# Optimization experiments

Hardware: AMD Instinct MI355X
Metric: run time of the kernel (lower is better)

Reference implementation:

```python
import jax, jax.numpy as jnp
import numpy as np

B, S, UNITS = 64, 2048, 1024


def setup_inputs() -> dict:
    key = jax.random.key(0)
    ks = jax.random.split(key, 6)
    scale = 1.0 / np.sqrt(UNITS)
    return {
        "s_prev": jax.random.normal(ks[0], (B, UNITS), dtype=jnp.float32),
        "hidden_states": jax.random.normal(ks[1], (B, S, UNITS), dtype=jnp.float32),
        "W_w": jax.random.normal(ks[2], (UNITS, UNITS), dtype=jnp.float32) * scale,
        "W_b": jnp.zeros((UNITS,), dtype=jnp.float32),
        "U_w": jax.random.normal(ks[3], (UNITS, UNITS), dtype=jnp.float32) * scale,
        "U_b": jnp.zeros((UNITS,), dtype=jnp.float32),
        "V_w": jax.random.normal(ks[4], (UNITS, 1), dtype=jnp.float32) * scale,
        "V_b": jnp.zeros((1,), dtype=jnp.float32),
    }


def reference(s_prev, hidden_states, W_w, W_b, U_w, U_b, V_w, V_b):
    # W(s_prev): [B, units] -> [B, 1, units]
    W_s = (s_prev @ W_w + W_b)[:, None, :]
    # U(hidden_states): [B, S, units]
    U_h = jnp.einsum('bsu,uk->bsk', hidden_states, U_w) + U_b
    # V(tanh(W_s + U_h)): [B, S, 1]
    scores = jnp.tanh(W_s + U_h) @ V_w + V_b
    # softmax over seq axis
    weights = jax.nn.softmax(scores, axis=1)  # [B, S, 1]
    # weighted sum over seq -> context [B, units]
    context = jnp.sum(weights * hidden_states, axis=1)
    return context, weights
```

## Files before the change

kernel.cpp:

```cpp
#include <hip/hip_runtime.h>

#define BB   64
#define SS   2048
#define UU   1024
#define MM   (BB * SS)

typedef unsigned short u16;
typedef unsigned int   u32;
typedef __attribute__((ext_vector_type(8))) short bf16x8;
typedef __attribute__((ext_vector_type(4))) float f32x4;

__device__ __forceinline__ u16 f2b(float f) {
    u32 x = __float_as_uint(f);
    u32 r = (x + 0x7fffu + ((x >> 16) & 1u)) >> 16;
    return (u16)r;
}
__device__ __forceinline__ float b2f(u16 u) {
    return __uint_as_float(((u32)u) << 16);
}
__device__ __forceinline__ float fast_tanh(float x) {
    x = fminf(fmaxf(x, -15.f), 15.f);
    float e = __expf(2.f * x);
    return (e - 1.f) / (e + 1.f);
}
__device__ __forceinline__ void async_copy16(const u16* gp, u16* lp) {
    __builtin_amdgcn_global_load_lds(
        (const __attribute__((address_space(1))) unsigned int*)gp,
        (__attribute__((address_space(3))) unsigned int*)lp, 16, 0, 0);
}

__global__ __launch_bounds__(256) void k_transpose_uw(const float* __restrict__ Uw,
                                                      u16* __restrict__ UwT) {
    __shared__ float tile[64][65];
    int n0 = blockIdx.x * 64, k0 = blockIdx.y * 64;
    int c = threadIdx.x & 63, r0 = threadIdx.x >> 6;
#pragma unroll
    for (int i = 0; i < 64; i += 4)
        tile[r0 + i][c] = Uw[(size_t)(k0 + r0 + i) * UU + n0 + c];
    __syncthreads();
#pragma unroll
    for (int i = 0; i < 64; i += 4)
        UwT[(size_t)(n0 + r0 + i) * UU + k0 + c] = f2b(tile[c][r0 + i]);
}

__global__ __launch_bounds__(256) void k_convert_h(const float* __restrict__ src,
                                                   u16* __restrict__ dst) {
    size_t i = ((size_t)blockIdx.x * 256 + threadIdx.x) * 8;
    float4 f0 = *(const float4*)(src + i);
    float4 f1 = *(const float4*)(src + i + 4);
    u16 t[8];
    t[0] = f2b(f0.x); t[1] = f2b(f0.y); t[2] = f2b(f0.z); t[3] = f2b(f0.w);
    t[4] = f2b(f1.x); t[5] = f2b(f1.y); t[6] = f2b(f1.z); t[7] = f2b(f1.w);
    *(uint4*)(dst + i) = *(uint4*)t;
}

__global__ __launch_bounds__(256) void k_ws(const float* __restrict__ sp,
                                            const float* __restrict__ Ww,
                                            const float* __restrict__ Wb,
                                            float* __restrict__ Ws) {
    int u = blockIdx.x * 256 + threadIdx.x;
    int b = blockIdx.y;
    int k0 = blockIdx.z * 256;
    const float* sprow = sp + (size_t)b * UU + k0;
    float acc = (blockIdx.z == 0) ? Wb[u] : 0.f;
#pragma unroll 4
    for (int k = 0; k < 256; ++k)
        acc = fmaf(sprow[k], Ww[(size_t)(k0 + k) * UU + u], acc);
    atomicAdd(&Ws[(size_t)b * UU + u], acc);
}

__global__ __launch_bounds__(256) void k_gemm_lds(const u16* __restrict__ A,
                                                  const u16* __restrict__ UwT,
                                                  const float* __restrict__ Ws,
                                                  const float* __restrict__ Ub,
                                                  const float* __restrict__ Vw,
                                                  float* __restrict__ scp) {
    __shared__ __align__(16) u16 As[128 * 64];
    __shared__ __align__(16) u16 Bs[128 * 64];
    const int tid  = threadIdx.x;
    const int lane = tid & 63;
    const int wave = tid >> 6;
    const int wm = wave >> 1, wn = wave & 1;
    const int quad = lane >> 4, l15 = lane & 15;

    const int bid = blockIdx.x;
    const int g   = bid >> 6;
    const int mt  = g * 8 + (bid & 7);
    const int nt  = (bid >> 3) & 7;
    const int n0  = nt * 128;
    const size_t m0 = (size_t)mt * 128;

    const int srow   = lane >> 3;
    const int schunk = (lane & 7) ^ srow;
    const size_t lane_off = (size_t)srow * UU + (size_t)schunk * 8;

    f32x4 acc[4][4];
#pragma unroll
    for (int i = 0; i < 4; ++i)
#pragma unroll
        for (int j = 0; j < 4; ++j) acc[i][j] = (f32x4){0.f, 0.f, 0.f, 0.f};

    for (int kk = 0; kk < UU; kk += 64) {
#pragma unroll
        for (int i = 0; i < 4; ++i) {
            const int gi = wave * 4 + i;
            async_copy16(A + (m0 + gi * 8) * UU + kk + lane_off, As + gi * 512);
        }
#pragma unroll
        for (int i = 0; i < 4; ++i) {
            const int gi = wave * 4 + i;
            async_copy16(UwT + (size_t)(n0 + gi * 8) * UU + kk + lane_off, Bs + gi * 512);
        }
        __syncthreads();
#pragma unroll
        for (int k2 = 0; k2 < 2; ++k2) {
            const int chunk = quad + k2 * 4;
            const int pos = chunk ^ (l15 & 7);
            bf16x8 a[4], b[4];
#pragma unroll
            for (int mi = 0; mi < 4; ++mi) {
                int r = wm * 64 + mi * 16 + l15;
                a[mi] = *(const bf16x8*)(As + r * 64 + pos * 8);
            }
#pragma unroll
            for (int ni = 0; ni < 4; ++ni) {
                int r = wn * 64 + ni * 16 + l15;
                b[ni] = *(const bf16x8*)(Bs + r * 64 + pos * 8);
            }
#pragma unroll
            for (int mi = 0; mi < 4; ++mi)
#pragma unroll
                for (int ni = 0; ni < 4; ++ni)
                    acc[mi][ni] = __builtin_amdgcn_mfma_f32_16x16x32_bf16(
                        a[mi], b[ni], acc[mi][ni], 0, 0, 0);
        }
        __syncthreads();
    }

    const int bidx = (int)(m0 >> 11);
    const float* wsrow = Ws + (size_t)bidx * UU;
    float wsv[4], ubv[4], vwv[4];
#pragma unroll
    for (int ni = 0; ni < 4; ++ni) {
        int ng = n0 + wn * 64 + ni * 16 + l15;
        wsv[ni] = wsrow[ng];
        ubv[ni] = Ub[ng];
        vwv[ni] = Vw[ng];
    }
#pragma unroll
    for (int mi = 0; mi < 4; ++mi) {
#pragma unroll
        for (int r = 0; r < 4; ++r) {
            float v = 0.f;
#pragma unroll
            for (int ni = 0; ni < 4; ++ni) {
                float x = acc[mi][ni][r] + wsv[ni] + ubv[ni];
                v = fmaf(fast_tanh(x), vwv[ni], v);
            }
#pragma unroll
            for (int off = 1; off < 16; off <<= 1)
                v += __shfl_xor(v, off, 64);
            if (l15 == 0) {
                size_t mg = m0 + wm * 64 + mi * 16 + quad * 4 + r;
                scp[mg * 16 + nt * 2 + wn] = v;
            }
        }
    }
}

__global__ __launch_bounds__(256) void k_gemm_f32(const float* __restrict__ Aptr,
                                                  const u16* __restrict__ UwT,
                                                  const float* __restrict__ Ws,
                                                  const float* __restrict__ Ub,
                                                  const float* __restrict__ Vw,
                                                  float* __restrict__ scp) {
    __shared__ __align__(16) u16 As[128][72];
    __shared__ __align__(16) u16 Bs[128][72];
    const int tid  = threadIdx.x;
    const int lane = tid & 63;
    const int wave = tid >> 6;
    const int wm = wave >> 1, wn = wave & 1;
    const int quad = lane >> 4, l15 = lane & 15;
    const int nt = blockIdx.x;
    const int n0 = nt * 128;
    const size_t m0 = (size_t)blockIdx.y * 128;

    f32x4 acc[4][4];
#pragma unroll
    for (int i = 0; i < 4; ++i)
#pragma unroll
        for (int j = 0; j < 4; ++j) acc[i][j] = (f32x4){0.f, 0.f, 0.f, 0.f};

    const int sr = tid >> 3;
    const int sc = (tid & 7) * 8;

    for (int kk = 0; kk < UU; kk += 64) {
#pragma unroll
        for (int i = 0; i < 4; ++i) {
            int r = sr + i * 32;
            const float4* p = (const float4*)(Aptr + (m0 + r) * UU + kk + sc);
            float4 f0 = p[0], f1 = p[1];
            u16 t[8];
            t[0] = f2b(f0.x); t[1] = f2b(f0.y); t[2] = f2b(f0.z); t[3] = f2b(f0.w);
            t[4] = f2b(f1.x); t[5] = f2b(f1.y); t[6] = f2b(f1.z); t[7] = f2b(f1.w);
            *(uint4*)(&As[r][sc]) = *(uint4*)t;
        }
#pragma unroll
        for (int i = 0; i < 4; ++i) {
            int r = sr + i * 32;
            uint4 v = *(const uint4*)(UwT + (size_t)(n0 + r) * UU + kk + sc);
            *(uint4*)(&Bs[r][sc]) = v;
        }
        __syncthreads();
#pragma unroll
        for (int k2 = 0; k2 < 64; k2 += 32) {
            bf16x8 a[4], b[4];
#pragma unroll
            for (int mi = 0; mi < 4; ++mi)
                a[mi] = *(const bf16x8*)(&As[wm * 64 + mi * 16 + l15][k2 + quad * 8]);
#pragma unroll
            for (int ni = 0; ni < 4; ++ni)
                b[ni] = *(const bf16x8*)(&Bs[wn * 64 + ni * 16 + l15][k2 + quad * 8]);
#pragma unroll
            for (int mi = 0; mi < 4; ++mi)
#pragma unroll
                for (int ni = 0; ni < 4; ++ni)
                    acc[mi][ni] = __builtin_amdgcn_mfma_f32_16x16x32_bf16(
                        a[mi], b[ni], acc[mi][ni], 0, 0, 0);
        }
        __syncthreads();
    }

    const int bidx = (int)(m0 >> 11);
    const float* wsrow = Ws + (size_t)bidx * UU;
    float wsv[4], ubv[4], vwv[4];
#pragma unroll
    for (int ni = 0; ni < 4; ++ni) {
        int ng = n0 + wn * 64 + ni * 16 + l15;
        wsv[ni] = wsrow[ng];
        ubv[ni] = Ub[ng];
        vwv[ni] = Vw[ng];
    }
#pragma unroll
    for (int mi = 0; mi < 4; ++mi) {
#pragma unroll
        for (int r = 0; r < 4; ++r) {
            float v = 0.f;
#pragma unroll
            for (int ni = 0; ni < 4; ++ni) {
                float x = acc[mi][ni][r] + wsv[ni] + ubv[ni];
                v = fmaf(fast_tanh(x), vwv[ni], v);
            }
#pragma unroll
            for (int off = 1; off < 16; off <<= 1)
                v += __shfl_xor(v, off, 64);
            if (l15 == 0) {
                size_t mg = m0 + wm * 64 + mi * 16 + quad * 4 + r;
                scp[mg * 16 + nt * 2 + wn] = v;
            }
        }
    }
}

__global__ __launch_bounds__(256) void k_softmax(const float* __restrict__ scp,
                                                 float* __restrict__ wout) {
    int b = blockIdx.x, t = threadIdx.x;
    __shared__ float red[256];
    float sc[8];
    float lmax = -1e30f;
#pragma unroll
    for (int i = 0; i < 8; ++i) {
        int s = t + i * 256;
        const float4* p = (const float4*)(scp + ((size_t)b * SS + s) * 16);
        float4 a = p[0], c = p[1], d = p[2], e = p[3];
        float v = (a.x + a.y + a.z + a.w) + (c.x + c.y + c.z + c.w) +
                  (d.x + d.y + d.z + d.w) + (e.x + e.y + e.z + e.w);
        sc[i] = v;
        lmax = fmaxf(lmax, v);
    }
    red[t] = lmax;
    __syncthreads();
    for (int o = 128; o > 0; o >>= 1) {
        if (t < o) red[t] = fmaxf(red[t], red[t + o]);
        __syncthreads();
    }
    float mx = red[0];
    __syncthreads();
    float lsum = 0.f;
#pragma unroll
    for (int i = 0; i < 8; ++i) {
        sc[i] = __expf(sc[i] - mx);
        lsum += sc[i];
    }
    red[t] = lsum;
    __syncthreads();
    for (int o = 128; o > 0; o >>= 1) {
        if (t < o) red[t] += red[t + o];
        __syncthreads();
    }
    float inv = 1.f / red[0];
#pragma unroll
    for (int i = 0; i < 8; ++i)
        wout[(size_t)b * SS + t + i * 256] = sc[i] * inv;
}

template <bool HBF16>
__global__ __launch_bounds__(256) void k_context(const void* __restrict__ hptr,
                                                 const float* __restrict__ w,
                                                 float* __restrict__ ctx) {
    int b = blockIdx.y;
    int s0 = blockIdx.x * 128;
    int u = threadIdx.x * 4;
    const float* wrow = w + (size_t)b * SS + s0;
    float a0 = 0.f, a1 = 0.f, a2 = 0.f, a3 = 0.f;
    for (int i = 0; i < 128; ++i) {
        float wv = wrow[i];
        size_t base = ((size_t)b * SS + s0 + i) * UU + u;
        if (HBF16) {
            ushort4 hv = *(const ushort4*)((const u16*)hptr + base);
            a0 = fmaf(wv, b2f(hv.x), a0);
            a1 = fmaf(wv, b2f(hv.y), a1);
            a2 = fmaf(wv, b2f(hv.z), a2);
            a3 = fmaf(wv, b2f(hv.w), a3);
        } else {
            float4 hv = *(const float4*)((const float*)hptr + base);
            a0 = fmaf(wv, hv.x, a0);
            a1 = fmaf(wv, hv.y, a1);
            a2 = fmaf(wv, hv.z, a2);
            a3 = fmaf(wv, hv.w, a3);
        }
    }
    atomicAdd(&ctx[(size_t)b * UU + u + 0], a0);
    atomicAdd(&ctx[(size_t)b * UU + u + 1], a1);
    atomicAdd(&ctx[(size_t)b * UU + u + 2], a2);
    atomicAdd(&ctx[(size_t)b * UU + u + 3], a3);
}

extern "C" void kernel_launch(void* const* d_in, const int* in_sizes, int n_in,
                              void* d_out, int out_size, void* d_ws, size_t ws_size,
                              hipStream_t stream) {
    const float* s_prev = (const float*)d_in[0];
    const float* h      = (const float*)d_in[1];
    const float* Ww     = (const float*)d_in[2];
    const float* Wb     = (const float*)d_in[3];
    const float* Uw     = (const float*)d_in[4];
    const float* Ub     = (const float*)d_in[5];
    const float* Vw     = (const float*)d_in[6];

    float* out = (float*)d_out;
    char* ws = (char*)d_ws;

    u16*   UwT = (u16*)ws;
    float* Ws  = (float*)(ws + (size_t)(2 << 20));
    float* scp = (float*)(ws + (size_t)(2 << 20) + (256 << 10));
    size_t offH = (size_t)(2 << 20) + (256 << 10) + ((size_t)8 << 20);
    u16*   hbf = (u16*)(ws + offH);
    const size_t hBytes = (size_t)MM * UU * 2;
    const bool useBf16 = (ws_size >= offH + hBytes);

    hipMemsetAsync(out, 0, (size_t)BB * UU * sizeof(float), stream);
    hipMemsetAsync(Ws, 0, (size_t)BB * UU * sizeof(float), stream);

    k_transpose_uw<<<dim3(16, 16), 256, 0, stream>>>(Uw, UwT);
    k_ws<<<dim3(4, BB, 4), 256, 0, stream>>>(s_prev, Ww, Wb, Ws);

    if (useBf16) {
        k_convert_h<<<(MM * (UU / 8)) / 256, 256, 0, stream>>>(h, hbf);
        k_gemm_lds<<<8192, 256, 0, stream>>>(hbf, UwT, Ws, Ub, Vw, scp);
    } else {
        k_gemm_f32<<<dim3(8, MM / 128), 256, 0, stream>>>(h, UwT, Ws, Ub, Vw, scp);
    }

    k_softmax<<<BB, 256, 0, stream>>>(scp, out + (size_t)BB * UU);

    if (useBf16)
        k_context<true><<<dim3(16, BB), 256, 0, stream>>>(hbf, out + (size_t)BB * UU, out);
    else
        k_context<false><<<dim3(16, BB), 256, 0, stream>>>(h, out + (size_t)BB * UU, out);
}
```

Baseline: 1.260 ms.

## Rewrite bf16 score GEMM as 256x256 tile with 4-stage async LDS pipeline

Replaces the 128x128 single-buffered GEMM with a 512-thread 256x256 tile kernel that uses a 4-deep ring of LDS buffers filled by async global-to-LDS copies, with explicit vmcnt waits and one barrier per k-step. Each wave now computes 128x64 of output. Blocks are remapped across XCDs, and the LDS swizzle is adapted to the 32-wide k chunks. The aim is to hide global load latency behind MFMA work and raise arithmetic intensity per loaded byte. The cost is much higher register and LDS use (128KB of LDS per block), which may limit occupancy.

```diff
diff --git a/kernel.cpp b/kernel.cpp
--- a/kernel.cpp
+++ b/kernel.cpp
@@ -28,6 +28,8 @@
         (const __attribute__((address_space(1))) unsigned int*)gp,
         (__attribute__((address_space(3))) unsigned int*)lp, 16, 0, 0);
 }
+
+#define WAITV(N) asm volatile("s_waitcnt vmcnt(" #N ")" ::: "memory")
 
 __global__ __launch_bounds__(256) void k_transpose_uw(const float* __restrict__ Uw,
                                                       u16* __restrict__ UwT) {
@@ -69,73 +71,96 @@
     atomicAdd(&Ws[(size_t)b * UU + u], acc);
 }
 
-__global__ __launch_bounds__(256) void k_gemm_lds(const u16* __restrict__ A,
-                                                  const u16* __restrict__ UwT,
-                                                  const float* __restrict__ Ws,
-                                                  const float* __restrict__ Ub,
-                                                  const float* __restrict__ Vw,
-                                                  float* __restrict__ scp) {
-    __shared__ __align__(16) u16 As[128 * 64];
-    __shared__ __align__(16) u16 Bs[128 * 64];
+__global__ __launch_bounds__(512, 2) void k_gemm256(const u16* __restrict__ A,
+                                                    const u16* __restrict__ UwT,
+                                                    const float* __restrict__ Ws,
+                                                    const float* __restrict__ Ub,
+                                                    const float* __restrict__ Vw,
+                                                    float* __restrict__ scp) {
+    __shared__ __align__(16) u16 As[4][8192];
+    __shared__ __align__(16) u16 Bs[4][8192];
     const int tid  = threadIdx.x;
     const int lane = tid & 63;
     const int wave = tid >> 6;
-    const int wm = wave >> 1, wn = wave & 1;
+    const int wm = wave >> 2;
+    const int wn = wave & 3;
     const int quad = lane >> 4, l15 = lane & 15;
 
     const int bid = blockIdx.x;
-    const int g   = bid >> 6;
-    const int mt  = g * 8 + (bid & 7);
-    const int nt  = (bid >> 3) & 7;
-    const int n0  = nt * 128;
-    const size_t m0 = (size_t)mt * 128;
-
-    const int srow   = lane >> 3;
-    const int schunk = (lane & 7) ^ srow;
+    const int xcd = bid & 7;
+    const int li  = bid >> 3;
+    const int mt  = xcd * 64 + (li >> 2);
+    const int nt  = li & 3;
+    const size_t m0 = (size_t)mt * 256;
+    const int n0  = nt * 256;
+
+    const int srow   = lane >> 2;
+    const int schunk = (lane & 3) ^ ((srow >> 1) & 3);
     const size_t lane_off = (size_t)srow * UU + (size_t)schunk * 8;
-
-    f32x4 acc[4][4];
-#pragma unroll
-    for (int i = 0; i < 4; ++i)
+    const int gA = wave * 2;
+
+    int offA[8], offB[4];
+#pragma unroll
+    for (int mi = 0; mi < 8; ++mi) {
+        int r = wm * 128 + mi * 16 + l15;
+        offA[mi] = r * 32 + (quad ^ ((r >> 1) & 3)) * 8;
+    }
+#pragma unroll
+    for (int ni = 0; ni < 4; ++ni) {
+        int r = wn * 64 + ni * 16 + l15;
+        offB[ni] = r * 32 + (quad ^ ((r >> 1) & 3)) * 8;
+    }
+
+    f32x4 acc[8][4];
+#pragma unroll
+    for (int i = 0; i < 8; ++i)
 #pragma unroll
         for (int j = 0; j < 4; ++j) acc[i][j] = (f32x4){0.f, 0.f, 0.f, 0.f};
 
-    for (int kk = 0; kk < UU; kk += 64) {
-#pragma unroll
-        for (int i = 0; i < 4; ++i) {
-            const int gi = wave * 4 + i;
-            async_copy16(A + (m0 + gi * 8) * UU + kk + lane_off, As + gi * 512);
-        }
-#pragma unroll
-        for (int i = 0; i < 4; ++i) {
-            const int gi = wave * 4 + i;
-            async_copy16(UwT + (size_t)(n0 + gi * 8) * UU + kk + lane_off, Bs + gi * 512);
-        }
-        __syncthreads();
-#pragma unroll
-        for (int k2 = 0; k2 < 2; ++k2) {
-            const int chunk = quad + k2 * 4;
-            const int pos = chunk ^ (l15 & 7);
-            bf16x8 a[4], b[4];
-#pragma unroll
-            for (int mi = 0; mi < 4; ++mi) {
-                int r = wm * 64 + mi * 16 + l15;
-                a[mi] = *(const bf16x8*)(As + r * 64 + pos * 8);
-            }
-#pragma unroll
-            for (int ni = 0; ni < 4; ++ni) {
-                int r = wn * 64 + ni * 16 + l15;
-                b[ni] = *(const bf16x8*)(Bs + r * 64 + pos * 8);
-            }
-#pragma unroll
-            for (int mi = 0; mi < 4; ++mi)
-#pragma unroll
-                for (int ni = 0; ni < 4; ++ni)
-                    acc[mi][ni] = __builtin_amdgcn_mfma_f32_16x16x32_bf16(
-                        a[mi], b[ni], acc[mi][ni], 0, 0, 0);
-        }
-        __syncthreads();
-    }
+    const u16* Abase = A + m0 * UU;
+    const u16* Bbase = UwT + (size_t)n0 * UU;
+
+#define STAGE(kt) do {                                                         \
+        const int _b = (kt) & 3;                                               \
+        const u16* _ga = Abase + (size_t)(gA * 16) * UU + (kt) * 32 + lane_off;\
+        async_copy16(_ga,                  &As[_b][gA * 512]);                 \
+        async_copy16(_ga + (size_t)16 * UU, &As[_b][(gA + 1) * 512]);          \
+        const u16* _gb = Bbase + (size_t)(gA * 16) * UU + (kt) * 32 + lane_off;\
+        async_copy16(_gb,                  &Bs[_b][gA * 512]);                 \
+        async_copy16(_gb + (size_t)16 * UU, &Bs[_b][(gA + 1) * 512]);          \
+    } while (0)
+
+    auto compute = [&](int kt) {
+        const u16* ab = As[kt & 3];
+        const u16* bb = Bs[kt & 3];
+        bf16x8 a[8], b[4];
+#pragma unroll
+        for (int mi = 0; mi < 8; ++mi) a[mi] = *(const bf16x8*)(ab + offA[mi]);
+#pragma unroll
+        for (int ni = 0; ni < 4; ++ni) b[ni] = *(const bf16x8*)(bb + offB[ni]);
+        __builtin_amdgcn_s_setprio(1);
+#pragma unroll
+        for (int mi = 0; mi < 8; ++mi)
+#pragma unroll
+            for (int ni = 0; ni < 4; ++ni)
+                acc[mi][ni] = __builtin_amdgcn_mfma_f32_16x16x32_bf16(
+                    a[mi], b[ni], acc[mi][ni], 0, 0, 0);
+        __builtin_amdgcn_s_setprio(0);
+    };
+
+    STAGE(0); STAGE(1); STAGE(2);
+
+    for (int kt = 0; kt < 29; ++kt) {
+        WAITV(8);
+        __builtin_amdgcn_sched_barrier(0);
+        __builtin_amdgcn_s_barrier();
+        STAGE(kt + 3);
+        compute(kt);
+    }
+    WAITV(8); __builtin_amdgcn_sched_barrier(0); __builtin_amdgcn_s_barrier(); compute(29);
+    WAITV(4); __builtin_amdgcn_sched_barrier(0); __builtin_amdgcn_s_barrier(); compute(30);
+    WAITV(0); __builtin_amdgcn_sched_barrier(0); __builtin_amdgcn_s_barrier(); compute(31);
+#undef STAGE
 
     const int bidx = (int)(m0 >> 11);
     const float* wsrow = Ws + (size_t)bidx * UU;
@@ -148,7 +173,7 @@
         vwv[ni] = Vw[ng];
     }
 #pragma unroll
-    for (int mi = 0; mi < 4; ++mi) {
+    for (int mi = 0; mi < 8; ++mi) {
 #pragma unroll
         for (int r = 0; r < 4; ++r) {
             float v = 0.f;
@@ -161,8 +186,8 @@
             for (int off = 1; off < 16; off <<= 1)
                 v += __shfl_xor(v, off, 64);
             if (l15 == 0) {
-                size_t mg = m0 + wm * 64 + mi * 16 + quad * 4 + r;
-                scp[mg * 16 + nt * 2 + wn] = v;
+                size_t mg = m0 + wm * 128 + mi * 16 + quad * 4 + r;
+                scp[mg * 16 + nt * 4 + wn] = v;
             }
         }
     }
@@ -366,7 +391,7 @@
 
     if (useBf16) {
         k_convert_h<<<(MM * (UU / 8)) / 256, 256, 0, stream>>>(h, hbf);
-        k_gemm_lds<<<8192, 256, 0, stream>>>(hbf, UwT, Ws, Ub, Vw, scp);
+        k_gemm256<<<2048, 512, 0, stream>>>(hbf, UwT, Ws, Ub, Vw, scp);
     } else {
         k_gemm_f32<<<dim3(8, MM / 128), 256, 0, stream>>>(h, UwT, Ws, Ub, Vw, scp);
     }
```

Measured after the change: 1.241 ms. No clear change (-1.5%).
